# Kernel tuning notes

Measured on AMD Instinct MI355X. Metric: run time of the kernel, lower is better.

Reference implementation:

```python
import jax, jax.numpy as jnp
import numpy as np

B, S, D = 32, 1024, 256
F_, K = 256, 3
T = 8192
LN_EPS = 1e-5


def _conv1d(x, w, b, padding):
    # x: [B, S, C_in], w: [C_out, C_in, K] -> [B, S, C_out]
    y = jax.lax.conv_general_dilated(
        x.transpose(0, 2, 1), w, window_strides=(1,),
        padding=[(padding, padding)], dimension_numbers=('NCH', 'OIH', 'NCH'))
    return y.transpose(0, 2, 1) + b


def _layernorm(x, g, b):
    mu = jnp.mean(x, axis=-1, keepdims=True)
    var = jnp.mean(jnp.square(x - mu), axis=-1, keepdims=True)
    return (x - mu) * jax.lax.rsqrt(var + LN_EPS) * g + b


def setup_inputs() -> dict:
    key = jax.random.key(0)
    ks = jax.random.split(key, 8)
    sc = 0.02
    return {
        'x': jax.random.normal(ks[0], (B, S, D), dtype=jnp.float32),
        'mask': jnp.zeros((B, S), dtype=bool),
        'duration': jax.random.randint(ks[1], (B, S), 0, 8, dtype=jnp.int32),
        'max_len': T,
        'conv1_w': jax.random.normal(ks[2], (F_, D, K), dtype=jnp.float32) * sc,
        'conv1_b': jnp.zeros((F_,), dtype=jnp.float32),
        'ln1_g': jnp.ones((F_,), dtype=jnp.float32),
        'ln1_b': jnp.zeros((F_,), dtype=jnp.float32),
        'conv2_w': jax.random.normal(ks[3], (F_, F_, K), dtype=jnp.float32) * sc,
        'conv2_b': jnp.zeros((F_,), dtype=jnp.float32),
        'ln2_g': jnp.ones((F_,), dtype=jnp.float32),
        'ln2_b': jnp.zeros((F_,), dtype=jnp.float32),
        'lin_w': jax.random.normal(ks[4], (F_, 1), dtype=jnp.float32) * sc,
        'lin_b': jnp.zeros((1,), dtype=jnp.float32),
    }


def reference(x, mask, duration, max_len, conv1_w, conv1_b, ln1_g, ln1_b,
              conv2_w, conv2_b, ln2_g, ln2_b, lin_w, lin_b):
    # ---- duration predictor (eval mode: dropout = identity) ----
    h = _conv1d(x, conv1_w, conv1_b, (K - 1) // 2)
    h = _layernorm(jax.nn.relu(h), ln1_g, ln1_b)
    h = _conv1d(h, conv2_w, conv2_b, 1)
    h = _layernorm(jax.nn.relu(h), ln2_g, ln2_b)
    log_dur = (h @ lin_w + lin_b)[..., 0]  # [B, S]
    log_dur = jnp.where(mask, 0.0, log_dur)

    # ---- length regulator: repeat_interleave + pad, done as one gather ----
    dur = duration.astype(jnp.int32)
    cum = jnp.cumsum(dur, axis=1)                                   # [B, S]
    t = jnp.arange(max_len, dtype=jnp.int32)                        # [T]
    src_idx = jax.vmap(lambda c: jnp.searchsorted(c, t, side='right'))(cum)  # [B, T]
    mel_len = jnp.minimum(cum[:, -1], max_len)                      # [B]
    valid = t[None, :] < mel_len[:, None]                           # [B, T]
    src_idx = jnp.clip(src_idx, 0, x.shape[1] - 1)
    out = jnp.take_along_axis(x, src_idx[:, :, None], axis=1)       # [B, T, D]
    out = jnp.where(valid[:, :, None], out, 0.0)
    # duration_target path -> duration_rounded = duration, mel_mask stays None
    return out, log_dur, dur, mel_len
```

## Files before the change

### kernel.cpp

```cpp
#include <hip/hip_runtime.h>
#include <cstddef>

constexpr int Bb   = 32;
constexpr int Ss   = 1024;
constexpr int Dd   = 256;
constexpr int Ff   = 256;
constexpr int TMAX = 8192;
constexpr int MM   = Bb * Ss;
constexpr int KK   = 768;
constexpr int SP   = 1026;
constexpr float LN_EPS = 1e-5f;
constexpr int PIT  = 72;

typedef __bf16 bf16x8 __attribute__((ext_vector_type(8)));
typedef __bf16 bf16x4 __attribute__((ext_vector_type(4)));
typedef float  f32x4  __attribute__((ext_vector_type(4)));

__global__ __launch_bounds__(256) void prep_k(
    const float* __restrict__ w1, const float* __restrict__ w2,
    __bf16* __restrict__ wTT1, __bf16* __restrict__ wTT2,
    const int* __restrict__ dur, float* __restrict__ dur_out,
    float* __restrict__ mel_out, int* __restrict__ idx,
    __bf16* __restrict__ xp2)
{
    __shared__ int ic[1024];
    __shared__ int sc[256];
    const int blk = blockIdx.x;
    const int tid = threadIdx.x;

    if (blk < 1536) {
        int i = blk * 256 + tid;
        const float* w = w1;
        __bf16* o = wTT1;
        int j = i;
        if (j >= Ff * KK) { j -= Ff * KK; w = w2; o = wTT2; }
        int d  = j & 255;
        int fk = j >> 8;
        int f  = fk / 3;
        int k  = fk - f * 3;
        o[(size_t)f * KK + k * 256 + d] = (__bf16)w[((size_t)(f * 256 + d)) * 3 + k];
        return;
    }
    if (blk >= 1568) {
        int j = (blk - 1568) * 256 + tid;
        int b = j >> 7;
        int r = (j >> 6) & 1;
        int d = (j & 63) * 4;
        *(bf16x4*)&xp2[((size_t)b * SP + (size_t)r * (SP - 1)) * 256 + d] =
            (bf16x4)(__bf16)0.f;
        return;
    }
    int b = blk - 1536;
    int4 d4 = ((const int4*)(dur + b * 1024))[tid];
    int l0 = d4.x, l1 = l0 + d4.y, l2 = l1 + d4.z, l3 = l2 + d4.w;
    sc[tid] = l3;
    __syncthreads();
    for (int off = 1; off < 256; off <<= 1) {
        int v = (tid >= off) ? sc[tid - off] : 0;
        __syncthreads();
        sc[tid] += v;
        __syncthreads();
    }
    int excl = sc[tid] - l3;
    ((int4*)ic)[tid] = make_int4(excl + l0, excl + l1, excl + l2, excl + l3);
    ((float4*)(dur_out + b * 1024))[tid] =
        make_float4((float)d4.x, (float)d4.y, (float)d4.z, (float)d4.w);
    if (tid == 255) mel_out[b] = (float)min(excl + l3, TMAX);
    __syncthreads();
    int mel = min(ic[1023], TMAX);
    for (int t = tid; t < TMAX; t += 256) {
        int lo = 0, hi = 1024;
        #pragma unroll
        for (int it = 0; it < 10; ++it) {
            int mid = (lo + hi) >> 1;
            if (ic[mid] <= t) lo = mid + 1; else hi = mid;
        }
        idx[b * TMAX + t] = (t < mel) ? min(lo, 1023) : -1;
    }
}

template<int MODE>
__global__ __launch_bounds__(512, 1) void gemm_fused(
    const float* __restrict__ Xf,
    const __bf16* __restrict__ Ap,
    const __bf16* __restrict__ Bw,
    const float* __restrict__ bias,
    const float* __restrict__ g, const float* __restrict__ bt,
    const float* __restrict__ lw, const float* __restrict__ lb,
    const unsigned char* __restrict__ mask,
    __bf16* __restrict__ outB, float* __restrict__ outF)
{
    __shared__ __bf16 As[128 * PIT];
    __shared__ __bf16 Bs[256 * PIT];

    const int tid  = threadIdx.x;
    const int m0   = blockIdx.x * 128;
    const int bb   = m0 >> 10;
    const int s0   = m0 & 1023;
    const int wave = tid >> 6;
    const int lane = tid & 63;
    const int wm   = (wave & 1) * 64;
    const int wn   = (wave >> 1) * 64;
    const int lm   = lane & 15;
    const int lk   = lane >> 4;

    f32x4 acc[4][4] = {};

    for (int step = 0; step < KK / 64; ++step) {
        const int kk0  = step * 64;
        const int kblk = kk0 >> 8;
        const int d0   = kk0 & 255;

        if constexpr (MODE == 0) {
            #pragma unroll
            for (int i = 0; i < 4; ++i) {
                int c = i * 512 + tid;
                int r = c >> 4, q = c & 15;
                int sg = s0 + r + kblk - 1;
                bf16x4 o = (bf16x4)(__bf16)0.f;
                if ((unsigned)sg < 1024u) {
                    float4 v = *(const float4*)&Xf[
                        (((size_t)(bb << 10) + sg) << 8) + d0 + q * 4];
                    o[0] = (__bf16)v.x; o[1] = (__bf16)v.y;
                    o[2] = (__bf16)v.z; o[3] = (__bf16)v.w;
                }
                *(bf16x4*)&As[r * PIT + q * 4] = o;
            }
        } else {
            const __bf16* aSrc = Ap + (((size_t)(bb * SP + s0 + kblk)) << 8) + d0;
            #pragma unroll
            for (int i = 0; i < 2; ++i) {
                int c = i * 512 + tid;
                int r = c >> 3, q = c & 7;
                *(bf16x8*)&As[r * PIT + q * 8] =
                    *(const bf16x8*)&aSrc[((size_t)r << 8) + q * 8];
            }
        }
        const __bf16* bSrc = Bw + kk0;
        #pragma unroll
        for (int i = 0; i < 4; ++i) {
            int c = i * 512 + tid;
            int r = c >> 3, q = c & 7;
            *(bf16x8*)&Bs[r * PIT + q * 8] =
                *(const bf16x8*)&bSrc[(size_t)r * KK + q * 8];
        }
        __syncthreads();

        #pragma unroll
        for (int kc = 0; kc < 2; ++kc) {
            bf16x8 af[4], bfr[4];
            #pragma unroll
            for (int mi = 0; mi < 4; ++mi)
                af[mi] = *(const bf16x8*)&As[(wm + mi * 16 + lm) * PIT + kc * 32 + lk * 8];
            #pragma unroll
            for (int ni = 0; ni < 4; ++ni)
                bfr[ni] = *(const bf16x8*)&Bs[(wn + ni * 16 + lm) * PIT + kc * 32 + lk * 8];
            #pragma unroll
            for (int mi = 0; mi < 4; ++mi)
                #pragma unroll
                for (int ni = 0; ni < 4; ++ni)
                    acc[mi][ni] = __builtin_amdgcn_mfma_f32_16x16x32_bf16(
                        af[mi], bfr[ni], acc[mi][ni], 0, 0, 0);
        }
        __syncthreads();
    }

    float* scrS = (float*)As;
    float* scrQ = scrS + 512;

    float s_[4][4] = {}, q_[4][4] = {};
    #pragma unroll
    for (int ni = 0; ni < 4; ++ni) {
        float bv = bias[wn + ni * 16 + lm];
        #pragma unroll
        for (int mi = 0; mi < 4; ++mi)
            #pragma unroll
            for (int r = 0; r < 4; ++r) {
                float h = fmaxf(acc[mi][ni][r] + bv, 0.f);
                acc[mi][ni][r] = h;
                s_[mi][r] += h;
                q_[mi][r] += h * h;
            }
    }
    #pragma unroll
    for (int off = 1; off < 16; off <<= 1)
        #pragma unroll
        for (int mi = 0; mi < 4; ++mi)
            #pragma unroll
            for (int r = 0; r < 4; ++r) {
                s_[mi][r] += __shfl_xor(s_[mi][r], off, 64);
                q_[mi][r] += __shfl_xor(q_[mi][r], off, 64);
            }
    if (lm == 0) {
        #pragma unroll
        for (int mi = 0; mi < 4; ++mi)
            #pragma unroll
            for (int r = 0; r < 4; ++r) {
                int rl = mi * 16 + lk * 4 + r;
                scrS[wave * 64 + rl] = s_[mi][r];
                scrQ[wave * 64 + rl] = q_[mi][r];
            }
    }
    __syncthreads();

    const int half = wave & 1;
    float mu[4][4], rs[4][4];
    #pragma unroll
    for (int mi = 0; mi < 4; ++mi)
        #pragma unroll
        for (int r = 0; r < 4; ++r) {
            int rl = mi * 16 + lk * 4 + r;
            float S = scrS[(0 + half) * 64 + rl] + scrS[(2 + half) * 64 + rl]
                    + scrS[(4 + half) * 64 + rl] + scrS[(6 + half) * 64 + rl];
            float Q = scrQ[(0 + half) * 64 + rl] + scrQ[(2 + half) * 64 + rl]
                    + scrQ[(4 + half) * 64 + rl] + scrQ[(6 + half) * 64 + rl];
            float m_ = S * (1.f / 256.f);
            float v_ = Q * (1.f / 256.f) - m_ * m_;
            mu[mi][r] = m_;
            rs[mi][r] = rsqrtf(v_ + LN_EPS);
        }

    if constexpr (MODE == 0) {
        size_t obase = ((size_t)(bb * SP + s0 + 1 + wm)) << 8;
        #pragma unroll
        for (int ni = 0; ni < 4; ++ni) {
            int col = wn + ni * 16 + lm;
            float gv = g[col], bv2 = bt[col];
            #pragma unroll
            for (int mi = 0; mi < 4; ++mi)
                #pragma unroll
                for (int r = 0; r < 4; ++r) {
                    int rl = mi * 16 + lk * 4 + r;
                    float o = (acc[mi][ni][r] - mu[mi][r]) * rs[mi][r] * gv + bv2;
                    outB[obase + ((size_t)rl << 8) + col] = (__bf16)o;
                }
        }
    } else {
        float p_[4][4] = {};
        #pragma unroll
        for (int ni = 0; ni < 4; ++ni) {
            int col = wn + ni * 16 + lm;
            float gv = g[col], bv2 = bt[col], wv = lw[col];
            #pragma unroll
            for (int mi = 0; mi < 4; ++mi)
                #pragma unroll
                for (int r = 0; r < 4; ++r) {
                    float o = (acc[mi][ni][r] - mu[mi][r]) * rs[mi][r] * gv + bv2;
                    p_[mi][r] += o * wv;
                }
        }
        #pragma unroll
        for (int off = 1; off < 16; off <<= 1)
            #pragma unroll
            for (int mi = 0; mi < 4; ++mi)
                #pragma unroll
                for (int r = 0; r < 4; ++r)
                    p_[mi][r] += __shfl_xor(p_[mi][r], off, 64);
        __syncthreads();
        if (lm == 0) {
            #pragma unroll
            for (int mi = 0; mi < 4; ++mi)
                #pragma unroll
                for (int r = 0; r < 4; ++r)
                    scrS[wave * 64 + (mi * 16 + lk * 4 + r)] = p_[mi][r];
        }
        __syncthreads();
        if (tid < 128) {
            int gr = tid;
            int h = gr >> 6, rl = gr & 63;
            float v = scrS[(0 + h) * 64 + rl] + scrS[(2 + h) * 64 + rl]
                    + scrS[(4 + h) * 64 + rl] + scrS[(6 + h) * 64 + rl] + lb[0];
            if (mask[m0 + gr]) v = 0.f;
            outF[m0 + gr] = v;
        }
    }
}

__global__ __launch_bounds__(256) void gather_k(
    const float4* __restrict__ xv, const int* __restrict__ idx,
    float4* __restrict__ outv)
{
    int g   = blockIdx.x * 256 + threadIdx.x;
    int row = g >> 6;
    int col = g & 63;
    int s = idx[row];
    float4 v = make_float4(0.f, 0.f, 0.f, 0.f);
    if (s >= 0) {
        int b = row >> 13;
        v = xv[((size_t)(b << 10) + s) * 64 + col];
    }
    outv[g] = v;
}

extern "C" void kernel_launch(void* const* d_in, const int* in_sizes, int n_in,
                              void* d_out, int out_size, void* d_ws, size_t ws_size,
                              hipStream_t stream)
{
    const float* x            = (const float*)d_in[0];
    const unsigned char* mask = (const unsigned char*)d_in[1];
    const int* duration       = (const int*)d_in[2];
    const float* w1  = (const float*)d_in[4];
    const float* b1  = (const float*)d_in[5];
    const float* g1  = (const float*)d_in[6];
    const float* be1 = (const float*)d_in[7];
    const float* w2  = (const float*)d_in[8];
    const float* b2  = (const float*)d_in[9];
    const float* g2  = (const float*)d_in[10];
    const float* be2 = (const float*)d_in[11];
    const float* lw  = (const float*)d_in[12];
    const float* lb  = (const float*)d_in[13];

    float* out        = (float*)d_out;
    float* out0       = out;
    float* out_logdur = out + (size_t)Bb * TMAX * Dd;
    float* out_dur    = out_logdur + (size_t)Bb * Ss;
    float* out_mel    = out_dur + (size_t)Bb * Ss;

    char* ws = (char*)d_ws;
    __bf16* xp2  = (__bf16*)ws;
    __bf16* wTT1 = xp2 + (size_t)Bb * SP * 256;
    __bf16* wTT2 = wTT1 + (size_t)Ff * KK;
    int*    idx  = (int*)(wTT2 + (size_t)Ff * KK);

    prep_k<<<1584, 256, 0, stream>>>(w1, w2, wTT1, wTT2,
                                     duration, out_dur, out_mel, idx, xp2);
    gemm_fused<0><<<MM / 128, 512, 0, stream>>>(
        x, nullptr, wTT1, b1, g1, be1, nullptr, nullptr, nullptr, xp2, nullptr);
    gemm_fused<1><<<MM / 128, 512, 0, stream>>>(
        nullptr, xp2, wTT2, b2, g2, be2, lw, lb, mask, nullptr, out_logdur);
    gather_k<<<(Bb * TMAX * Dd / 4) / 256, 256, 0, stream>>>(
        (const float4*)x, idx, (float4*)out0);
}
```

Baseline: 384.0 us.

## Fuse gather into GEMM kernels and shrink GEMM tile to 64 rows

Removes the separate gather kernel and appends its work as extra blocks to each of the two GEMM launches, half in each, so the memory-bound gather can overlap with the compute-bound GEMM blocks. The GEMM tile shrinks from 128x256 with 512 threads to 64x256 with 256 threads, and launch bounds allow 3 blocks per CU, which raises the GEMM block count and occupancy. The cost is more reloading of weight tiles per output row, plus many small gather blocks sharing the GEMM's launch configuration and register budget.

```diff
diff --git a/kernel.cpp b/kernel.cpp
--- a/kernel.cpp
+++ b/kernel.cpp
@@ -11,6 +11,10 @@
 constexpr int SP   = 1026;
 constexpr float LN_EPS = 1e-5f;
 constexpr int PIT  = 72;
+
+constexpr int GEMM_BLK = MM / 64;
+constexpr int GATH_TOT = Bb * TMAX * Dd / 4 / 256;
+constexpr int GATH_HALF = GATH_TOT / 2;
 
 typedef __bf16 bf16x8 __attribute__((ext_vector_type(8)));
 typedef __bf16 bf16x4 __attribute__((ext_vector_type(4)));
@@ -80,7 +84,7 @@
 }
 
 template<int MODE>
-__global__ __launch_bounds__(512, 1) void gemm_fused(
+__global__ __launch_bounds__(256, 3) void gemm_fused(
     const float* __restrict__ Xf,
     const __bf16* __restrict__ Ap,
     const __bf16* __restrict__ Bw,
@@ -88,19 +92,35 @@
     const float* __restrict__ g, const float* __restrict__ bt,
     const float* __restrict__ lw, const float* __restrict__ lb,
     const unsigned char* __restrict__ mask,
-    __bf16* __restrict__ outB, float* __restrict__ outF)
+    __bf16* __restrict__ outB, float* __restrict__ outF,
+    const int* __restrict__ idx, float4* __restrict__ outv)
 {
-    __shared__ __bf16 As[128 * PIT];
+    __shared__ __bf16 As[64 * PIT];
     __shared__ __bf16 Bs[256 * PIT];
 
-    const int tid  = threadIdx.x;
-    const int m0   = blockIdx.x * 128;
+    const int tid = threadIdx.x;
+
+    if (blockIdx.x >= GEMM_BLK) {
+        int gblk = blockIdx.x - GEMM_BLK + MODE * GATH_HALF;
+        int gg   = gblk * 256 + tid;
+        int row  = gg >> 6;
+        int col  = gg & 63;
+        int s = idx[row];
+        float4 v = make_float4(0.f, 0.f, 0.f, 0.f);
+        if (s >= 0) {
+            int b = row >> 13;
+            v = ((const float4*)Xf)[((size_t)(b << 10) + s) * 64 + col];
+        }
+        outv[gg] = v;
+        return;
+    }
+
+    const int m0   = blockIdx.x * 64;
     const int bb   = m0 >> 10;
     const int s0   = m0 & 1023;
     const int wave = tid >> 6;
     const int lane = tid & 63;
-    const int wm   = (wave & 1) * 64;
-    const int wn   = (wave >> 1) * 64;
+    const int wn   = wave * 64;
     const int lm   = lane & 15;
     const int lk   = lane >> 4;
 
@@ -114,7 +134,7 @@
         if constexpr (MODE == 0) {
             #pragma unroll
             for (int i = 0; i < 4; ++i) {
-                int c = i * 512 + tid;
+                int c = i * 256 + tid;
                 int r = c >> 4, q = c & 15;
                 int sg = s0 + r + kblk - 1;
                 bf16x4 o = (bf16x4)(__bf16)0.f;
@@ -130,28 +150,25 @@
             const __bf16* aSrc = Ap + (((size_t)(bb * SP + s0 + kblk)) << 8) + d0;
             #pragma unroll
             for (int i = 0; i < 2; ++i) {
-                int c = i * 512 + tid;
-                int r = c >> 3, q = c & 7;
+                int c = i * 256 + tid, r = c >> 3, q = c & 7;
                 *(bf16x8*)&As[r * PIT + q * 8] =
                     *(const bf16x8*)&aSrc[((size_t)r << 8) + q * 8];
             }
         }
         const __bf16* bSrc = Bw + kk0;
         #pragma unroll
-        for (int i = 0; i < 4; ++i) {
-            int c = i * 512 + tid;
-            int r = c >> 3, q = c & 7;
+        for (int i = 0; i < 8; ++i) {
+            int c = i * 256 + tid, r = c >> 3, q = c & 7;
             *(bf16x8*)&Bs[r * PIT + q * 8] =
                 *(const bf16x8*)&bSrc[(size_t)r * KK + q * 8];
         }
         __syncthreads();
-
         #pragma unroll
         for (int kc = 0; kc < 2; ++kc) {
             bf16x8 af[4], bfr[4];
             #pragma unroll
             for (int mi = 0; mi < 4; ++mi)
-                af[mi] = *(const bf16x8*)&As[(wm + mi * 16 + lm) * PIT + kc * 32 + lk * 8];
+                af[mi] = *(const bf16x8*)&As[(mi * 16 + lm) * PIT + kc * 32 + lk * 8];
             #pragma unroll
             for (int ni = 0; ni < 4; ++ni)
                 bfr[ni] = *(const bf16x8*)&Bs[(wn + ni * 16 + lm) * PIT + kc * 32 + lk * 8];
@@ -166,7 +183,7 @@
     }
 
     float* scrS = (float*)As;
-    float* scrQ = scrS + 512;
+    float* scrQ = scrS + 256;
 
     float s_[4][4] = {}, q_[4][4] = {};
     #pragma unroll
@@ -196,24 +213,21 @@
         for (int mi = 0; mi < 4; ++mi)
             #pragma unroll
             for (int r = 0; r < 4; ++r) {
-                int rl = mi * 16 + lk * 4 + r;
-                scrS[wave * 64 + rl] = s_[mi][r];
-                scrQ[wave * 64 + rl] = q_[mi][r];
+                int row = mi * 16 + lk * 4 + r;
+                scrS[wave * 64 + row] = s_[mi][r];
+                scrQ[wave * 64 + row] = q_[mi][r];
             }
     }
     __syncthreads();
 
-    const int half = wave & 1;
     float mu[4][4], rs[4][4];
     #pragma unroll
     for (int mi = 0; mi < 4; ++mi)
         #pragma unroll
         for (int r = 0; r < 4; ++r) {
-            int rl = mi * 16 + lk * 4 + r;
-            float S = scrS[(0 + half) * 64 + rl] + scrS[(2 + half) * 64 + rl]
-                    + scrS[(4 + half) * 64 + rl] + scrS[(6 + half) * 64 + rl];
-            float Q = scrQ[(0 + half) * 64 + rl] + scrQ[(2 + half) * 64 + rl]
-                    + scrQ[(4 + half) * 64 + rl] + scrQ[(6 + half) * 64 + rl];
+            int row = mi * 16 + lk * 4 + r;
+            float S = scrS[row] + scrS[64 + row] + scrS[128 + row] + scrS[192 + row];
+            float Q = scrQ[row] + scrQ[64 + row] + scrQ[128 + row] + scrQ[192 + row];
             float m_ = S * (1.f / 256.f);
             float v_ = Q * (1.f / 256.f) - m_ * m_;
             mu[mi][r] = m_;
@@ -221,7 +235,7 @@
         }
 
     if constexpr (MODE == 0) {
-        size_t obase = ((size_t)(bb * SP + s0 + 1 + wm)) << 8;
+        size_t obase = ((size_t)(bb * SP + s0 + 1)) << 8;
         #pragma unroll
         for (int ni = 0; ni < 4; ++ni) {
             int col = wn + ni * 16 + lm;
@@ -230,9 +244,9 @@
             for (int mi = 0; mi < 4; ++mi)
                 #pragma unroll
                 for (int r = 0; r < 4; ++r) {
-                    int rl = mi * 16 + lk * 4 + r;
+                    int row = mi * 16 + lk * 4 + r;
                     float o = (acc[mi][ni][r] - mu[mi][r]) * rs[mi][r] * gv + bv2;
-                    outB[obase + ((size_t)rl << 8) + col] = (__bf16)o;
+                    outB[obase + ((size_t)row << 8) + col] = (__bf16)o;
                 }
         }
     } else {
@@ -265,31 +279,14 @@
                     scrS[wave * 64 + (mi * 16 + lk * 4 + r)] = p_[mi][r];
         }
         __syncthreads();
-        if (tid < 128) {
-            int gr = tid;
-            int h = gr >> 6, rl = gr & 63;
-            float v = scrS[(0 + h) * 64 + rl] + scrS[(2 + h) * 64 + rl]
-                    + scrS[(4 + h) * 64 + rl] + scrS[(6 + h) * 64 + rl] + lb[0];
-            if (mask[m0 + gr]) v = 0.f;
-            outF[m0 + gr] = v;
-        }
-    }
-}
-
-__global__ __launch_bounds__(256) void gather_k(
-    const float4* __restrict__ xv, const int* __restrict__ idx,
-    float4* __restrict__ outv)
-{
-    int g   = blockIdx.x * 256 + threadIdx.x;
-    int row = g >> 6;
-    int col = g & 63;
-    int s = idx[row];
-    float4 v = make_float4(0.f, 0.f, 0.f, 0.f);
-    if (s >= 0) {
-        int b = row >> 13;
-        v = xv[((size_t)(b << 10) + s) * 64 + col];
-    }
-    outv[g] = v;
+        if (tid < 64) {
+            int row = tid;
+            float v = scrS[row] + scrS[64 + row] + scrS[128 + row] + scrS[192 + row]
+                      + lb[0];
+            if (mask[m0 + row]) v = 0.f;
+            outF[m0 + row] = v;
+        }
+    }
 }
 
 extern "C" void kernel_launch(void* const* d_in, const int* in_sizes, int n_in,
@@ -324,10 +321,10 @@
 
     prep_k<<<1584, 256, 0, stream>>>(w1, w2, wTT1, wTT2,
                                      duration, out_dur, out_mel, idx, xp2);
-    gemm_fused<0><<<MM / 128, 512, 0, stream>>>(
-        x, nullptr, wTT1, b1, g1, be1, nullptr, nullptr, nullptr, xp2, nullptr);
-    gemm_fused<1><<<MM / 128, 512, 0, stream>>>(
-        nullptr, xp2, wTT2, b2, g2, be2, lw, lb, mask, nullptr, out_logdur);
-    gather_k<<<(Bb * TMAX * Dd / 4) / 256, 256, 0, stream>>>(
-        (const float4*)x, idx, (float4*)out0);
+    gemm_fused<0><<<GEMM_BLK + GATH_HALF, 256, 0, stream>>>(
+        x, nullptr, wTT1, b1, g1, be1, nullptr, nullptr, nullptr,
+        xp2, nullptr, idx, (float4*)out0);
+    gemm_fused<1><<<GEMM_BLK + GATH_HALF, 256, 0, stream>>>(
+        x, xp2, wTT2, b2, g2, be2, lw, lb, mask,
+        nullptr, out_logdur, idx, (float4*)out0);
 }
```

Measured after the change: 388.2 us. No clear change (+1.1%).
